# Kernel tuning notes

Hardware: AMD Instinct MI355X
Metric: run time of the kernel (lower is better)

The kernel has to match this reference:

```python
import jax, jax.numpy as jnp
import numpy as np

EMB = 1024
HEAD = 128

def setup_inputs() -> dict:
    key = jax.random.key(0)
    kx, kk, kq, kv = jax.random.split(key, 4)
    s = 1.0 / np.sqrt(EMB)
    return {
        "x": jax.random.normal(kx, (8, 2048, EMB), dtype=jnp.float32),
        "Wk": jax.random.normal(kk, (EMB, HEAD), dtype=jnp.float32) * s,
        "Wq": jax.random.normal(kq, (EMB, HEAD), dtype=jnp.float32) * s,
        "Wv": jax.random.normal(kv, (EMB, HEAD), dtype=jnp.float32) * s,
    }

def reference(x, Wk, Wq, Wv):
    # x: [B,T,E]; projections (no bias)
    k = jnp.einsum('bte,eh->bth', x, Wk)
    q = jnp.einsum('bte,eh->bth', x, Wq)
    v = jnp.einsum('bte,eh->bth', x, Wv)
    # scores: [B,T,T], NOTE: no 1/sqrt(d) scaling in original module
    qk = jnp.einsum('bih,bjh->bij', q, k)
    T = x.shape[1]
    causal = jnp.tril(jnp.ones((T, T), dtype=bool))  # True = keep
    qk = jnp.where(causal, qk, -jnp.inf)
    # NOTE: softmax over axis -2 (query axis), as in original
    attn = jax.nn.softmax(qk, axis=-2)
    return jnp.einsum('bij,bjh->bih', attn, v)
```

## Files before the change

kernel.cpp:

```cpp
#include <hip/hip_runtime.h>

typedef unsigned short u16;
typedef unsigned int u32;
typedef _Float16 f16;
typedef __attribute__((ext_vector_type(8))) _Float16 f16x8;
typedef __attribute__((ext_vector_type(4))) float f32x4;
typedef __attribute__((ext_vector_type(16))) float f32x16;

constexpr int SEQ = 2048;
constexpr int EMBD = 1024;
constexpr int HD = 128;
constexpr int NB = 8;
constexpr int NSLS = 8;
constexpr int NSLP = 8;

__device__ inline u16 f2h(float f) { return __builtin_bit_cast(u16, (f16)f); }
__device__ inline u32 pack2(float a, float b) { return (u32)f2h(a) | ((u32)f2h(b) << 16); }

__device__ inline f32x4 mfma16(f16x8 a, f16x8 b, f32x4 c) {
  return __builtin_amdgcn_mfma_f32_16x16x32_f16(a, b, c, 0, 0, 0);
}
__device__ inline f32x16 mfma32(f16x8 a, f16x8 b, f32x16 c) {
  return __builtin_amdgcn_mfma_f32_32x32x16_f16(a, b, c, 0, 0, 0);
}

__device__ __forceinline__ void gload16(const u16* g, u16* l) {
  __builtin_amdgcn_global_load_lds(
      (const __attribute__((address_space(1))) u32*)g,
      (__attribute__((address_space(3))) u32*)l, 16, 0, 0);
}

template<int RB>
__device__ inline f16x8 frag_ld(const u16* lds, int row, int e) {
  int byte = row * RB + ((e * 2) ^ ((row & 7) << 4));
  return *reinterpret_cast<const f16x8*>(reinterpret_cast<const char*>(lds) + byte);
}

__global__ __launch_bounds__(256) void k_cvt_w(const float* __restrict__ Wq,
                                               const float* __restrict__ Wk,
                                               const float* __restrict__ Wv,
                                               u16* __restrict__ Wt) {
  int t = blockIdx.x * 256 + threadIdx.x;
  int e0 = (t & 255) * 4;
  int H = t >> 8;
  int w = H >> 7, h = H & 127;
  const float* W = (w == 0) ? Wq : (w == 1) ? Wk : Wv;
  ushort4 o;
  o.x = f2h(W[(size_t)(e0 + 0) * HD + h]);
  o.y = f2h(W[(size_t)(e0 + 1) * HD + h]);
  o.z = f2h(W[(size_t)(e0 + 2) * HD + h]);
  o.w = f2h(W[(size_t)(e0 + 3) * HD + h]);
  int k0t = e0 >> 6, ec = e0 & 63;
  size_t el = (size_t)(k0t * 384 + H) * 64 + (ec ^ ((H & 7) << 3));
  *reinterpret_cast<ushort4*>(Wt + el) = o;
}

__global__ __launch_bounds__(512, 4) void k_proj(const float* __restrict__ x,
                                                 const u16* __restrict__ Wt,
                                                 u16* __restrict__ Qb,
                                                 u16* __restrict__ Kb,
                                                 u16* __restrict__ Vtb) {
  __shared__ __align__(16) u16 As[2][64 * 64];
  __shared__ __align__(16) u16 Bs[2][192 * 64];
  const int mt = blockIdx.x, ny = blockIdx.y;
  const int t = threadIdx.x, lane = t & 63, wave = t >> 6;
  const int rh = (wave & 1) * 32, cq = (wave >> 1) * 48;
  const int ar = t >> 3, ac = t & 7;
  const float* asrc = x + (size_t)(mt * 64 + ar) * EMBD + ac * 8;
  const int adst = ar * 64 + ((ac * 8) ^ ((ar & 7) << 3));
  f32x4 zero = {0.f, 0.f, 0.f, 0.f};
  f32x4 acc[2][3];
#pragma unroll
  for (int a = 0; a < 2; ++a)
#pragma unroll
    for (int b = 0; b < 3; ++b) acc[a][b] = zero;

  float4 xe0, xe1, xo0, xo1;
  xe0 = *reinterpret_cast<const float4*>(asrc);
  xe1 = *reinterpret_cast<const float4*>(asrc + 4);
#pragma unroll
  for (int q = 0; q < 3; ++q) {
    int lin = q * 512 + t;
    gload16(Wt + ny * 12288 + lin * 8, &Bs[0][lin * 8]);
  }
  {
    uint4 o = {pack2(xe0.x, xe0.y), pack2(xe0.z, xe0.w), pack2(xe1.x, xe1.y), pack2(xe1.z, xe1.w)};
    *reinterpret_cast<uint4*>(&As[0][adst]) = o;
  }
  xo0 = *reinterpret_cast<const float4*>(asrc + 64);
  xo1 = *reinterpret_cast<const float4*>(asrc + 68);
  __syncthreads();
#pragma unroll 2
  for (int s = 0; s < 16; ++s) {
    const int cur = s & 1;
    if (s + 1 < 16) {
#pragma unroll
      for (int q = 0; q < 3; ++q) {
        int lin = q * 512 + t;
        gload16(Wt + (s + 1) * 24576 + ny * 12288 + lin * 8, &Bs[cur ^ 1][lin * 8]);
      }
    }
    if (s + 2 < 16) {
      if (cur == 0) {
        xe0 = *reinterpret_cast<const float4*>(asrc + (s + 2) * 64);
        xe1 = *reinterpret_cast<const float4*>(asrc + (s + 2) * 64 + 4);
      } else {
        xo0 = *reinterpret_cast<const float4*>(asrc + (s + 2) * 64);
        xo1 = *reinterpret_cast<const float4*>(asrc + (s + 2) * 64 + 4);
      }
    }
    __builtin_amdgcn_s_setprio(1);
#pragma unroll
    for (int kk = 0; kk < 2; ++kk) {
      f16x8 af0 = frag_ld<128>(As[cur], rh + (lane & 15), kk * 32 + (lane >> 4) * 8);
      f16x8 af1 = frag_ld<128>(As[cur], rh + 16 + (lane & 15), kk * 32 + (lane >> 4) * 8);
#pragma unroll
      for (int fc = 0; fc < 3; ++fc) {
        f16x8 bw = frag_ld<128>(Bs[cur], cq + fc * 16 + (lane & 15), kk * 32 + (lane >> 4) * 8);
        acc[0][fc] = mfma16(af0, bw, acc[0][fc]);
        acc[1][fc] = mfma16(af1, bw, acc[1][fc]);
      }
    }
    __builtin_amdgcn_s_setprio(0);
    if (s + 1 < 16) {
      uint4 o;
      if (cur == 0)
        o = {pack2(xo0.x, xo0.y), pack2(xo0.z, xo0.w), pack2(xo1.x, xo1.y), pack2(xo1.z, xo1.w)};
      else
        o = {pack2(xe0.x, xe0.y), pack2(xe0.z, xe0.w), pack2(xe1.x, xe1.y), pack2(xe1.z, xe1.w)};
      *reinterpret_cast<uint4*>(&As[cur ^ 1][adst]) = o;
    }
    __syncthreads();
  }
#pragma unroll
  for (int fi = 0; fi < 2; ++fi)
#pragma unroll
    for (int fc = 0; fc < 3; ++fc) {
      int gcol = ny * 192 + cq + fc * 16 + (lane & 15);
      int w = gcol >> 7, h = gcol & 127;
      int i0 = mt * 64 + rh + fi * 16 + (lane >> 4) * 4;
      if (w < 2) {
        u16* P = w ? Kb : Qb;
#pragma unroll
        for (int r = 0; r < 4; ++r) {
          int i = i0 + r;
          P[(size_t)i * 128 + (h ^ ((i & 7) << 3))] = f2h(acc[fi][fc][r]);
        }
      } else {
        int bb = i0 >> 11, jt = (i0 >> 6) & 31, tl = i0 & 63;
        ushort4 o = {f2h(acc[fi][fc][0]), f2h(acc[fi][fc][1]),
                     f2h(acc[fi][fc][2]), f2h(acc[fi][fc][3])};
        size_t el = ((size_t)(bb * 32 + jt) * 128 + h) * 64 + (tl ^ ((h & 7) << 3));
        *reinterpret_cast<ushort4*>(Vtb + el) = o;
      }
    }
}

__device__ inline void merge_ml(float& m, float& l, float m2, float l2) {
  float mn = fmaxf(m, m2);
  float a = (m > -1e37f) ? l * __expf(m - mn) : 0.f;
  float b = (m2 > -1e37f) ? l2 * __expf(m2 - mn) : 0.f;
  m = mn;
  l = a + b;
}

__global__ __launch_bounds__(256, 2) void k_statsA(const u16* __restrict__ Qb,
                                                   const u16* __restrict__ Kb,
                                                   float* __restrict__ mpart,
                                                   float* __restrict__ lpart) {
  __shared__ __align__(16) u16 Qs[2][128 * 128];
  const int id = blockIdx.x;
  const int bb = id & 7, z = (id >> 3) & 7, sl = id >> 6;
  const int t = threadIdx.x, lane = t & 63, wj = (t >> 6) * 32;
  f32x4 zero = {0.f, 0.f, 0.f, 0.f};

  for (int ph = 0; ph < 2; ++ph) {
    const int jt = ph ? 15 - z : z;
    __syncthreads();
#pragma unroll
    for (int q = 0; q < 8; ++q) {
      int lin = q * 256 + t;
      gload16(Kb + ((size_t)bb * SEQ + jt * 128) * 128 + lin * 8, &Qs[0][lin * 8]);
    }
    __syncthreads();
    f16x8 af[2][4];
#pragma unroll
    for (int fj = 0; fj < 2; ++fj)
#pragma unroll
      for (int kk = 0; kk < 4; ++kk)
        af[fj][kk] = frag_ld<256>(Qs[0], wj + fj * 16 + (lane & 15), kk * 32 + (lane >> 4) * 8);
    float m[2][4], l[2][4];
#pragma unroll
    for (int a = 0; a < 2; ++a)
#pragma unroll
      for (int r = 0; r < 4; ++r) {
        m[a][r] = -INFINITY;
        l[a][r] = 0.f;
      }
    const int it0 = jt + ((sl - jt) & 7);
    int cur = 1;
    if (it0 < 16) {
#pragma unroll
      for (int q = 0; q < 8; ++q) {
        int lin = q * 256 + t;
        gload16(Qb + ((size_t)bb * SEQ + it0 * 128) * 128 + lin * 8, &Qs[1][lin * 8]);
      }
      for (int it = it0; it < 16; it += 8) {
        __syncthreads();
        if (it + 8 < 16) {
#pragma unroll
          for (int q = 0; q < 8; ++q) {
            int lin = q * 256 + t;
            gload16(Qb + ((size_t)bb * SEQ + (it + 8) * 128) * 128 + lin * 8,
                    &Qs[cur ^ 1][lin * 8]);
          }
        }
        f32x4 acc[2][8];
#pragma unroll
        for (int a = 0; a < 2; ++a)
#pragma unroll
          for (int b = 0; b < 8; ++b) acc[a][b] = zero;
        __builtin_amdgcn_s_setprio(1);
#pragma unroll
        for (int kk = 0; kk < 4; ++kk)
#pragma unroll
          for (int fi = 0; fi < 8; ++fi) {
            f16x8 bq = frag_ld<256>(Qs[cur], fi * 16 + (lane & 15), kk * 32 + (lane >> 4) * 8);
            acc[0][fi] = mfma16(af[0][kk], bq, acc[0][fi]);
            acc[1][fi] = mfma16(af[1][kk], bq, acc[1][fi]);
          }
        __builtin_amdgcn_s_setprio(0);
        if (it == jt) {
#pragma unroll
          for (int fj = 0; fj < 2; ++fj)
#pragma unroll
            for (int r = 0; r < 4; ++r) {
              int jg = jt * 128 + wj + fj * 16 + (lane >> 4) * 4 + r;
              float v[8];
              float vmax = -INFINITY;
#pragma unroll
              for (int fi = 0; fi < 8; ++fi) {
                int ig = it * 128 + fi * 16 + (lane & 15);
                v[fi] = (ig >= jg) ? acc[fj][fi][r] : -INFINITY;
                vmax = fmaxf(vmax, v[fi]);
              }
              if (vmax > -1e37f) {
                float mn = fmaxf(m[fj][r], vmax);
                float sc = (m[fj][r] > -1e37f) ? __expf(m[fj][r] - mn) : 0.f;
                float ss = 0.f;
#pragma unroll
                for (int fi = 0; fi < 8; ++fi)
                  ss += (v[fi] > -1e37f) ? __expf(v[fi] - mn) : 0.f;
                l[fj][r] = l[fj][r] * sc + ss;
                m[fj][r] = mn;
              }
            }
        } else {
#pragma unroll
          for (int fj = 0; fj < 2; ++fj)
#pragma unroll
            for (int r = 0; r < 4; ++r) {
              float vmax = acc[fj][0][r];
#pragma unroll
              for (int fi = 1; fi < 8; ++fi) vmax = fmaxf(vmax, acc[fj][fi][r]);
              float mn = fmaxf(m[fj][r], vmax);
              float sc = __expf(m[fj][r] - mn);
              float ss = 0.f;
#pragma unroll
              for (int fi = 0; fi < 8; ++fi) ss += __expf(acc[fj][fi][r] - mn);
              l[fj][r] = l[fj][r] * sc + ss;
              m[fj][r] = mn;
            }
        }
        cur ^= 1;
      }
    }
#pragma unroll
    for (int fj = 0; fj < 2; ++fj)
#pragma unroll
      for (int r = 0; r < 4; ++r)
        for (int msk = 1; msk <= 8; msk <<= 1) {
          float m2 = __shfl_xor(m[fj][r], msk);
          float l2 = __shfl_xor(l[fj][r], msk);
          merge_ml(m[fj][r], l[fj][r], m2, l2);
        }
    if ((lane & 15) == 0) {
#pragma unroll
      for (int fj = 0; fj < 2; ++fj)
#pragma unroll
        for (int r = 0; r < 4; ++r) {
          int j = jt * 128 + wj + fj * 16 + (lane >> 4) * 4 + r;
          size_t idx = (size_t)sl * (NB * SEQ) + (size_t)bb * SEQ + j;
          mpart[idx] = m[fj][r];
          lpart[idx] = l[fj][r];
        }
    }
  }
}

__global__ __launch_bounds__(256) void k_stats_reduce(const float* __restrict__ mpart,
                                                      const float* __restrict__ lpart,
                                                      float* __restrict__ Cg) {
  int idx = blockIdx.x * 256 + threadIdx.x;
  float m = -INFINITY;
#pragma unroll
  for (int sl = 0; sl < NSLS; sl++) m = fmaxf(m, mpart[sl * (NB * SEQ) + idx]);
  float l = 0.f;
#pragma unroll
  for (int sl = 0; sl < NSLS; sl++) {
    float ms = mpart[sl * (NB * SEQ) + idx];
    if (ms > -1e37f) l += lpart[sl * (NB * SEQ) + idx] * __expf(ms - m);
  }
  Cg[idx] = m + __logf(l);
}

__global__ __launch_bounds__(256, 2) void k_passB(const u16* __restrict__ Qb,
                                                  const u16* __restrict__ Kb,
                                                  const u16* __restrict__ Vtb,
                                                  const float* __restrict__ Cg,
                                                  u16* __restrict__ opart) {
  __shared__ __align__(16) u16 Ks2[2][64 * 128];
  __shared__ __align__(16) u16 Vs2[2][128 * 64];
  __shared__ __align__(16) u16 Ps[128 * 64];
  const int id = blockIdx.x;
  const int bb = id & 7, z = (id >> 3) & 7, sl = id >> 6;
  const int t = threadIdx.x, lane = t & 63, wave = t >> 6;
  const int l31 = lane & 31, lh = lane >> 5;

  auto stageKV = [&](int jt, int b) {
#pragma unroll
    for (int q = 0; q < 4; ++q) {
      int lin = q * 256 + t;
      gload16(Kb + ((size_t)bb * SEQ + jt * 64) * 128 + lin * 8, &Ks2[b][lin * 8]);
    }
#pragma unroll
    for (int q = 0; q < 4; ++q) {
      int lin = q * 256 + t;
      gload16(Vtb + ((size_t)bb * 32 + jt) * 8192 + lin * 8, &Vs2[b][lin * 8]);
    }
  };

  for (int ph = 0; ph < 2; ++ph) {
    const int it = ph ? 15 - z : z;
    f16x8 qa[8];
    {
      size_t gi = (size_t)bb * SEQ + it * 128 + wave * 32 + l31;
      const u16* qrow = Qb + gi * 128;
      int sw = ((int)gi & 7) << 3;
#pragma unroll
      for (int ks = 0; ks < 8; ++ks) {
        int e0 = ks * 16 + lh * 8;
        qa[ks] = *reinterpret_cast<const f16x8*>(qrow + (e0 ^ sw));
      }
    }
    f32x16 accO[4];
#pragma unroll
    for (int b = 0; b < 4; ++b)
#pragma unroll
      for (int q = 0; q < 16; ++q) accO[b][q] = 0.f;
    const int jtmax = 2 * it + 1;
    __syncthreads();
    if (sl <= jtmax) stageKV(sl, 0);
    int cur = 0;
    for (int jt = sl; jt <= jtmax; jt += NSLP) {
      __syncthreads();
      if (jt + NSLP <= jtmax) stageKV(jt + NSLP, cur ^ 1);
      float cj[2];
#pragma unroll
      for (int jtile = 0; jtile < 2; ++jtile)
        cj[jtile] = Cg[bb * SEQ + jt * 64 + jtile * 32 + l31];
      f32x16 accS[2];
#pragma unroll
      for (int b = 0; b < 2; ++b)
#pragma unroll
        for (int q = 0; q < 16; ++q) accS[b][q] = 0.f;
      __builtin_amdgcn_s_setprio(1);
#pragma unroll
      for (int ks = 0; ks < 8; ++ks)
#pragma unroll
        for (int jtile = 0; jtile < 2; ++jtile) {
          f16x8 bk = frag_ld<256>(Ks2[cur], jtile * 32 + l31, ks * 16 + lh * 8);
          accS[jtile] = mfma32(qa[ks], bk, accS[jtile]);
        }
      __builtin_amdgcn_s_setprio(0);
#pragma unroll
      for (int jtile = 0; jtile < 2; ++jtile) {
        int jloc = jtile * 32 + l31;
        int jg = jt * 64 + jloc;
        float c = cj[jtile];
#pragma unroll
        for (int q = 0; q < 16; ++q) {
          int iloc = wave * 32 + (q & 3) + 8 * (q >> 2) + 4 * lh;
          int ig = it * 128 + iloc;
          float p = __expf(accS[jtile][q] - c);
          if (ig < jg) p = 0.f;
          Ps[iloc * 64 + (jloc ^ ((iloc & 7) << 3))] = f2h(p);
        }
      }
      __builtin_amdgcn_s_setprio(1);
#pragma unroll
      for (int js = 0; js < 4; ++js) {
        f16x8 pa = frag_ld<128>(Ps, wave * 32 + l31, js * 16 + lh * 8);
#pragma unroll
        for (int sh = 0; sh < 4; ++sh) {
          f16x8 bv = frag_ld<128>(Vs2[cur], sh * 32 + l31, js * 16 + lh * 8);
          accO[sh] = mfma32(pa, bv, accO[sh]);
        }
      }
      __builtin_amdgcn_s_setprio(0);
      cur ^= 1;
    }
#pragma unroll
    for (int sh = 0; sh < 4; ++sh) {
      int h = sh * 32 + l31;
#pragma unroll
      for (int q = 0; q < 16; ++q) {
        int ig = it * 128 + wave * 32 + (q & 3) + 8 * (q >> 2) + 4 * lh;
        opart[(((size_t)sl * NB + bb) * SEQ + ig) * HD + h] = f2h(accO[sh][q]);
      }
    }
  }
}

__global__ __launch_bounds__(256) void k_reduceB(const u16* __restrict__ opart,
                                                 float* __restrict__ out) {
  size_t base = ((size_t)blockIdx.x * 256 + threadIdx.x) * 8;
  const size_t S = (size_t)NB * SEQ * HD;
  float s[8];
#pragma unroll
  for (int j = 0; j < 8; j++) s[j] = 0.f;
#pragma unroll
  for (int sl = 0; sl < NSLP; sl++) {
    f16x8 v = *reinterpret_cast<const f16x8*>(opart + sl * S + base);
#pragma unroll
    for (int j = 0; j < 8; j++) s[j] += (float)v[j];
  }
  float4 o0 = {s[0], s[1], s[2], s[3]};
  float4 o1 = {s[4], s[5], s[6], s[7]};
  *reinterpret_cast<float4*>(out + base) = o0;
  *reinterpret_cast<float4*>(out + base + 4) = o1;
}

extern "C" void kernel_launch(void* const* d_in, const int* in_sizes, int n_in,
                              void* d_out, int out_size, void* d_ws, size_t ws_size,
                              hipStream_t stream) {
  (void)in_sizes; (void)n_in; (void)out_size; (void)ws_size;
  const float* x = (const float*)d_in[0];
  const float* Wk = (const float*)d_in[1];
  const float* Wq = (const float*)d_in[2];
  const float* Wv = (const float*)d_in[3];
  float* out = (float*)d_out;
  char* ws = (char*)d_ws;

  u16* Wt = (u16*)(ws + 0);
  u16* Qb = (u16*)(ws + 786432);
  u16* Kb = (u16*)(ws + 4980736);
  u16* Vtb = (u16*)(ws + 9175040);
  float* mpart = (float*)(ws + 13369344);
  float* lpart = (float*)(ws + 13893632);
  float* Cg = (float*)(ws + 14417920);
  u16* opart = (u16*)(ws + 14548992);

  k_cvt_w<<<384, 256, 0, stream>>>(Wq, Wk, Wv, Wt);
  k_proj<<<dim3(256, 2), 512, 0, stream>>>(x, Wt, Qb, Kb, Vtb);
  k_statsA<<<512, 256, 0, stream>>>(Qb, Kb, mpart, lpart);
  k_stats_reduce<<<64, 256, 0, stream>>>(mpart, lpart, Cg);
  k_passB<<<512, 256, 0, stream>>>(Qb, Kb, Vtb, Cg, opart);
  k_reduceB<<<1024, 256, 0, stream>>>(opart, out);
}
```

Measured before the change: 80.77 us.

## Fold softmax normalizer into QK MFMA and keep P in registers

After: 84.44 us. +4.5%, slower.

```diff
diff --git a/kernel.cpp b/kernel.cpp
--- a/kernel.cpp
+++ b/kernel.cpp
@@ -22,6 +22,14 @@
 }
 __device__ inline f32x16 mfma32(f16x8 a, f16x8 b, f32x16 c) {
   return __builtin_amdgcn_mfma_f32_32x32x16_f16(a, b, c, 0, 0, 0);
+}
+
+__device__ inline u32 pkrtz(float a, float b) {
+  auto t = __builtin_amdgcn_cvt_pkrtz(a, b);
+  return __builtin_bit_cast(u32, t);
+}
+__device__ inline void plswap(u32& a, u32& b) {
+  asm volatile("v_permlane32_swap_b32 %0, %1" : "+v"(a), "+v"(b));
 }
 
 __device__ __forceinline__ void gload16(const u16* g, u16* l) {
@@ -300,7 +308,8 @@
 
 __global__ __launch_bounds__(256) void k_stats_reduce(const float* __restrict__ mpart,
                                                       const float* __restrict__ lpart,
-                                                      float* __restrict__ Cg) {
+                                                      const u16* __restrict__ Kb,
+                                                      u16* __restrict__ Kxb) {
   int idx = blockIdx.x * 256 + threadIdx.x;
   float m = -INFINITY;
 #pragma unroll
@@ -311,17 +320,28 @@
     float ms = mpart[sl * (NB * SEQ) + idx];
     if (ms > -1e37f) l += lpart[sl * (NB * SEQ) + idx] * __expf(ms - m);
   }
-  Cg[idx] = m + __logf(l);
+  float negC = -(m + __logf(l));
+  f16 hi = (f16)negC;
+  f16 lo = (f16)(negC - (float)hi);
+  const uint4* src = reinterpret_cast<const uint4*>(Kb + (size_t)idx * 128);
+  uint4* dst = reinterpret_cast<uint4*>(Kxb + (size_t)idx * 160);
+#pragma unroll
+  for (int q = 0; q < 16; ++q) dst[q] = src[q];
+  uint4 ext = {(u32)__builtin_bit_cast(u16, hi) | ((u32)__builtin_bit_cast(u16, lo) << 16),
+               0u, 0u, 0u};
+  uint4 z4 = {0u, 0u, 0u, 0u};
+  dst[16] = ext;
+  dst[17] = z4;
+  dst[18] = z4;
+  dst[19] = z4;
 }
 
 __global__ __launch_bounds__(256, 2) void k_passB(const u16* __restrict__ Qb,
-                                                  const u16* __restrict__ Kb,
+                                                  const u16* __restrict__ Kxb,
                                                   const u16* __restrict__ Vtb,
-                                                  const float* __restrict__ Cg,
                                                   u16* __restrict__ opart) {
-  __shared__ __align__(16) u16 Ks2[2][64 * 128];
+  __shared__ __align__(16) u16 Ks2[2][64 * 160];
   __shared__ __align__(16) u16 Vs2[2][128 * 64];
-  __shared__ __align__(16) u16 Ps[128 * 64];
   const int id = blockIdx.x;
   const int bb = id & 7, z = (id >> 3) & 7, sl = id >> 6;
   const int t = threadIdx.x, lane = t & 63, wave = t >> 6;
@@ -329,9 +349,9 @@
 
   auto stageKV = [&](int jt, int b) {
 #pragma unroll
-    for (int q = 0; q < 4; ++q) {
+    for (int q = 0; q < 5; ++q) {
       int lin = q * 256 + t;
-      gload16(Kb + ((size_t)bb * SEQ + jt * 64) * 128 + lin * 8, &Ks2[b][lin * 8]);
+      gload16(Kxb + ((size_t)bb * SEQ + jt * 64) * 160 + lin * 8, &Ks2[b][lin * 8]);
     }
 #pragma unroll
     for (int q = 0; q < 4; ++q) {
@@ -339,6 +359,12 @@
       gload16(Vtb + ((size_t)bb * 32 + jt) * 8192 + lin * 8, &Vs2[b][lin * 8]);
     }
   };
+
+  f16x8 qext = {};
+  if (lh == 0) {
+    qext[0] = (f16)1.f;
+    qext[1] = (f16)1.f;
+  }
 
   for (int ph = 0; ph < 2; ++ph) {
     const int it = ph ? 15 - z : z;
@@ -348,10 +374,8 @@
       const u16* qrow = Qb + gi * 128;
       int sw = ((int)gi & 7) << 3;
 #pragma unroll
-      for (int ks = 0; ks < 8; ++ks) {
-        int e0 = ks * 16 + lh * 8;
-        qa[ks] = *reinterpret_cast<const f16x8*>(qrow + (e0 ^ sw));
-      }
+      for (int ks = 0; ks < 8; ++ks)
+        qa[ks] = *reinterpret_cast<const f16x8*>(qrow + ((ks * 16 + lh * 8) ^ sw));
     }
     f32x16 accO[4];
 #pragma unroll
@@ -359,16 +383,13 @@
 #pragma unroll
       for (int q = 0; q < 16; ++q) accO[b][q] = 0.f;
     const int jtmax = 2 * it + 1;
+    const int ig = it * 128 + wave * 32 + l31;
     __syncthreads();
     if (sl <= jtmax) stageKV(sl, 0);
     int cur = 0;
     for (int jt = sl; jt <= jtmax; jt += NSLP) {
       __syncthreads();
       if (jt + NSLP <= jtmax) stageKV(jt + NSLP, cur ^ 1);
-      float cj[2];
-#pragma unroll
-      for (int jtile = 0; jtile < 2; ++jtile)
-        cj[jtile] = Cg[bb * SEQ + jt * 64 + jtile * 32 + l31];
       f32x16 accS[2];
 #pragma unroll
       for (int b = 0; b < 2; ++b)
@@ -379,34 +400,49 @@
       for (int ks = 0; ks < 8; ++ks)
 #pragma unroll
         for (int jtile = 0; jtile < 2; ++jtile) {
-          f16x8 bk = frag_ld<256>(Ks2[cur], jtile * 32 + l31, ks * 16 + lh * 8);
-          accS[jtile] = mfma32(qa[ks], bk, accS[jtile]);
-        }
+          f16x8 bk = frag_ld<320>(Ks2[cur], jtile * 32 + l31, ks * 16 + lh * 8);
+          accS[jtile] = mfma32(bk, qa[ks], accS[jtile]);
+        }
+#pragma unroll
+      for (int jtile = 0; jtile < 2; ++jtile) {
+        f16x8 bk8 = *reinterpret_cast<const f16x8*>(
+            reinterpret_cast<const char*>(Ks2[cur]) + (jtile * 32 + l31) * 320 + 256 + lh * 16);
+        accS[jtile] = mfma32(bk8, qext, accS[jtile]);
+      }
       __builtin_amdgcn_s_setprio(0);
+      f16x8 pa[4];
 #pragma unroll
       for (int jtile = 0; jtile < 2; ++jtile) {
-        int jloc = jtile * 32 + l31;
-        int jg = jt * 64 + jloc;
-        float c = cj[jtile];
+        float p[16];
 #pragma unroll
         for (int q = 0; q < 16; ++q) {
-          int iloc = wave * 32 + (q & 3) + 8 * (q >> 2) + 4 * lh;
-          int ig = it * 128 + iloc;
-          float p = __expf(accS[jtile][q] - c);
-          if (ig < jg) p = 0.f;
-          Ps[iloc * 64 + (jloc ^ ((iloc & 7) << 3))] = f2h(p);
+          int jg = jt * 64 + jtile * 32 + (q & 3) + 8 * (q >> 2) + 4 * lh;
+          p[q] = (ig >= jg) ? __expf(accS[jtile][q]) : 0.f;
+        }
+        u32 W[4][2];
+#pragma unroll
+        for (int g = 0; g < 4; ++g) {
+          W[g][0] = pkrtz(p[4 * g + 0], p[4 * g + 1]);
+          W[g][1] = pkrtz(p[4 * g + 2], p[4 * g + 3]);
+        }
+#pragma unroll
+        for (int s = 0; s < 2; ++s) {
+          u32 a0 = W[2 * s][0], b0 = W[2 * s + 1][0];
+          u32 a1 = W[2 * s][1], b1 = W[2 * s + 1][1];
+          plswap(a0, b0);
+          plswap(a1, b1);
+          uint4 words = {a0, a1, b0, b1};
+          pa[jtile * 2 + s] = __builtin_bit_cast(f16x8, words);
         }
       }
       __builtin_amdgcn_s_setprio(1);
 #pragma unroll
-      for (int js = 0; js < 4; ++js) {
-        f16x8 pa = frag_ld<128>(Ps, wave * 32 + l31, js * 16 + lh * 8);
+      for (int js = 0; js < 4; ++js)
 #pragma unroll
         for (int sh = 0; sh < 4; ++sh) {
           f16x8 bv = frag_ld<128>(Vs2[cur], sh * 32 + l31, js * 16 + lh * 8);
-          accO[sh] = mfma32(pa, bv, accO[sh]);
-        }
-      }
+          accO[sh] = mfma32(pa[js], bv, accO[sh]);
+        }
       __builtin_amdgcn_s_setprio(0);
       cur ^= 1;
     }
@@ -415,8 +451,8 @@
       int h = sh * 32 + l31;
 #pragma unroll
       for (int q = 0; q < 16; ++q) {
-        int ig = it * 128 + wave * 32 + (q & 3) + 8 * (q >> 2) + 4 * lh;
-        opart[(((size_t)sl * NB + bb) * SEQ + ig) * HD + h] = f2h(accO[sh][q]);
+        int ig2 = it * 128 + wave * 32 + (q & 3) + 8 * (q >> 2) + 4 * lh;
+        opart[(((size_t)sl * NB + bb) * SEQ + ig2) * HD + h] = f2h(accO[sh][q]);
       }
     }
   }
@@ -456,15 +492,15 @@
   u16* Qb = (u16*)(ws + 786432);
   u16* Kb = (u16*)(ws + 4980736);
   u16* Vtb = (u16*)(ws + 9175040);
-  float* mpart = (float*)(ws + 13369344);
-  float* lpart = (float*)(ws + 13893632);
-  float* Cg = (float*)(ws + 14417920);
-  u16* opart = (u16*)(ws + 14548992);
+  u16* Kxb = (u16*)(ws + 13369344);
+  float* mpart = (float*)(ws + 18612224);
+  float* lpart = (float*)(ws + 19136512);
+  u16* opart = (u16*)(ws + 19660800);
 
   k_cvt_w<<<384, 256, 0, stream>>>(Wq, Wk, Wv, Wt);
   k_proj<<<dim3(256, 2), 512, 0, stream>>>(x, Wt, Qb, Kb, Vtb);
   k_statsA<<<512, 256, 0, stream>>>(Qb, Kb, mpart, lpart);
-  k_stats_reduce<<<64, 256, 0, stream>>>(mpart, lpart, Cg);
-  k_passB<<<512, 256, 0, stream>>>(Qb, Kb, Vtb, Cg, opart);
+  k_stats_reduce<<<64, 256, 0, stream>>>(mpart, lpart, Kb, Kxb);
+  k_passB<<<512, 256, 0, stream>>>(Qb, Kxb, Vtb, opart);
   k_reduceB<<<1024, 256, 0, stream>>>(opart, out);
 }
```
